# Kernel optimization log

Measured on AMD Instinct MI355X. Metric: run time of the kernel, lower is better.

The kernel has to match this reference:

```python
import jax, jax.numpy as jnp
import numpy as np

V, E, H2, T = 50000, 256, 512, 16  # vocab, embed, hidden_dim, tagset
H = H2 // 2                        # per-direction hidden
START, STOP = 14, 15
NEG = -10000.0


def setup_inputs() -> dict:
    key = jax.random.key(0)
    ks = jax.random.split(key, 13)
    s = 0.08
    tokens = jax.random.randint(ks[0], (32, 512), 0, V)
    embed_table = jax.random.normal(ks[1], (V, E), jnp.float32)
    Wi_f = jax.random.normal(ks[2], (4 * H, E), jnp.float32) * s
    Wh_f = jax.random.normal(ks[3], (4 * H, H), jnp.float32) * s
    bi_f = jnp.zeros((4 * H,), jnp.float32)
    bh_f = jnp.zeros((4 * H,), jnp.float32)
    Wi_b = jax.random.normal(ks[4], (4 * H, E), jnp.float32) * s
    Wh_b = jax.random.normal(ks[5], (4 * H, H), jnp.float32) * s
    bi_b = jnp.zeros((4 * H,), jnp.float32)
    bh_b = jnp.zeros((4 * H,), jnp.float32)
    Wt = jax.random.normal(ks[6], (T, H2), jnp.float32) * s
    bt = jnp.zeros((T,), jnp.float32)
    trans = jax.random.normal(ks[7], (T, T), jnp.float32)
    trans = trans.at[START, :].set(NEG).at[:, STOP].set(NEG)
    return {"tokens": tokens, "embed_table": embed_table,
            "Wi_f": Wi_f, "Wh_f": Wh_f, "bi_f": bi_f, "bh_f": bh_f,
            "Wi_b": Wi_b, "Wh_b": Wh_b, "bi_b": bi_b, "bh_b": bh_b,
            "Wt": Wt, "bt": bt, "transitions": trans}


def _lstm_dir(x, Wi, Wh, bi, bh, reverse=False):
    # x: [S, B, E] -> h seq [S, B, H], PyTorch gate order i,f,g,o
    S, B, _ = x.shape
    xs = x[::-1] if reverse else x
    pre = jnp.einsum('sbe,ge->sbg', xs, Wi) + bi + bh  # precompute input GEMM

    def step(carry, z_t):
        h, c = carry
        z = z_t + h @ Wh.T  # [B, 4H]
        i, f, g, o = jnp.split(z, 4, axis=-1)
        c = jax.nn.sigmoid(f) * c + jax.nn.sigmoid(i) * jnp.tanh(g)
        h = jax.nn.sigmoid(o) * jnp.tanh(c)
        return (h, c), h

    h0 = jnp.zeros((B, H), x.dtype)
    _, hs = jax.lax.scan(step, (h0, h0), pre)
    return hs[::-1] if reverse else hs


def reference(tokens, embed_table, Wi_f, Wh_f, bi_f, bh_f,
              Wi_b, Wh_b, bi_b, bh_b, Wt, bt, transitions):
    x = embed_table[tokens]                # [B, S, E]
    x = jnp.transpose(x, (1, 0, 2))        # [S, B, E] seq-first like nn.LSTM
    hf = _lstm_dir(x, Wi_f, Wh_f, bi_f, bh_f, reverse=False)
    hb = _lstm_dir(x, Wi_b, Wh_b, bi_b, bh_b, reverse=True)
    feats = jnp.concatenate([hf, hb], axis=-1)           # [S, B, 2H]
    emissions = jnp.einsum('sbh,th->sbt', feats, Wt) + bt  # [S, B, T]

    B = tokens.shape[0]
    alpha0 = jnp.full((B, T), NEG, jnp.float32).at[:, START].set(0.0)

    def crf_step(alpha, emit_t):
        # alpha: [B, T_prev]; transitions[next, prev]; emit_t: [B, T_next]
        scores = alpha[:, None, :] + transitions[None, :, :] + emit_t[:, :, None]
        return jax.nn.logsumexp(scores, axis=2), None

    alpha, _ = jax.lax.scan(crf_step, alpha0, emissions)
    log_Z = jax.nn.logsumexp(alpha + transitions[STOP][None, :], axis=1)  # [B]
    return log_Z
```

## Files before the change

kernel.cpp:

```cpp
#include <hip/hip_runtime.h>
#include <hip/hip_bf16.h>
#include <stdint.h>

typedef __attribute__((ext_vector_type(4))) float f32x4;
typedef __attribute__((ext_vector_type(8))) short bf16x8;

#define SENT 0xFFFFFFFFFFFFFFFFULL

#define WS_XBF   0u
#define WS_WIR   8388608u
#define WS_BIAS  9437184u
#define WS_PRE   9445376u
#define WS_HALL  76554240u
#define WS_CTL   93364224u
#define WS_EMIS  93368320u
#define WS_CHK   94416896u

__device__ __forceinline__ unsigned short f2bf(float x) {
    union { float f; unsigned int u; } v; v.f = x;
    return (unsigned short)((v.u + 0x7FFFu + ((v.u >> 16) & 1u)) >> 16);
}
__device__ __forceinline__ float bf2f(unsigned short b) {
    union { float f; unsigned int u; } v; v.u = ((unsigned int)b) << 16; return v.f;
}
__device__ __forceinline__ unsigned int pack2(float a, float b) {
    return (unsigned int)f2bf(a) | ((unsigned int)f2bf(b) << 16);
}
__device__ __forceinline__ float sigf(float x)  { return 1.0f / (1.0f + __expf(-x)); }
__device__ __forceinline__ float tanhf_(float x){ return 1.0f - 2.0f / (__expf(2.0f * x) + 1.0f); }

__global__ __launch_bounds__(256) void k_prep(
    const int* __restrict__ tokens, const float* __restrict__ embed,
    const float* __restrict__ Wi_f, const float* __restrict__ Wi_b,
    const float* __restrict__ bi_f, const float* __restrict__ bh_f,
    const float* __restrict__ bi_b, const float* __restrict__ bh_b,
    char* __restrict__ ws)
{
    int blk = blockIdx.x, tid = threadIdx.x;
    unsigned short* xbf  = (unsigned short*)(ws + WS_XBF);
    unsigned short* wir  = (unsigned short*)(ws + WS_WIR);
    float* biasr         = (float*)(ws + WS_BIAS);
    if (blk < 2048) {
        int rr = tid >> 5, cc = tid & 31;
        int r = blk * 8 + rr;
        int s = r >> 5, b = r & 31;
        int tok = tokens[b * 512 + s];
        int k = cc * 8;
        const float* src = embed + (size_t)tok * 256 + k;
        float4 a = *(const float4*)src;
        float4 c = *(const float4*)(src + 4);
        uint4 o; o.x = pack2(a.x, a.y); o.y = pack2(a.z, a.w);
        o.z = pack2(c.x, c.y); o.w = pack2(c.z, c.w);
        *(uint4*)(xbf + (size_t)r * 256 + k) = o;
    } else if (blk < 2304) {
        int rr = tid >> 5, cc = tid & 31;
        int rowp = (blk - 2048) * 8 + rr;
        int dir = rowp >> 10, q = rowp & 1023;
        int j = q >> 8, rs = q & 255;
        int g = rs >> 6, hl = rs & 63;
        int srow = g * 256 + j * 64 + hl;
        const float* W = dir ? Wi_b : Wi_f;
        int k = cc * 8;
        const float* src = W + (size_t)srow * 256 + k;
        float4 a = *(const float4*)src;
        float4 c = *(const float4*)(src + 4);
        uint4 o; o.x = pack2(a.x, a.y); o.y = pack2(a.z, a.w);
        o.z = pack2(c.x, c.y); o.w = pack2(c.z, c.w);
        *(uint4*)(wir + (size_t)rowp * 256 + k) = o;
        if (cc == 0)
            biasr[rowp] = dir ? (bi_b[srow] + bh_b[srow]) : (bi_f[srow] + bh_f[srow]);
    } else {
        if (blk == 2304 && tid < 16)
            ((unsigned int*)(ws + WS_CTL))[tid] = 0u;
        size_t g = (size_t)(blk - 2304) * 256 + tid;
        uint4* hall4 = (uint4*)(ws + WS_HALL);
        const unsigned int NF = 0xFFFFFFFFu;
        for (size_t u = g; u < 1050624u; u += 65536u) {
            size_t slot = (u >> 10) % 513u;
            uint4 val;
            if (slot == 0) { val.x = 0u; val.y = 0u; val.z = 0u; val.w = 0u; }
            else           { val.x = NF; val.y = NF; val.z = NF; val.w = NF; }
            hall4[u] = val;
        }
    }
}

__global__ __launch_bounds__(256) void k_pregemm(char* __restrict__ ws)
{
    __shared__ unsigned short Asb[128 * 136];
    __shared__ unsigned short Bsb[64 * 136];
    const unsigned short* xbf = (const unsigned short*)(ws + WS_XBF);
    const unsigned short* wir = (const unsigned short*)(ws + WS_WIR);
    const float* biasr        = (const float*)(ws + WS_BIAS);
    unsigned short* pre       = (unsigned short*)(ws + WS_PRE);
    int blk = blockIdx.x, tid = threadIdx.x;
    int mb = blk >> 5, nb = blk & 31;
    int Mbase = mb * 128, Nbase = nb * 64;
    int w = tid >> 6, l = tid & 63, col = l & 15, quad = l >> 4;
    f32x4 acc[4][2];
    #pragma unroll
    for (int a = 0; a < 4; ++a)
        #pragma unroll
        for (int b = 0; b < 2; ++b) acc[a][b] = (f32x4){0.f, 0.f, 0.f, 0.f};

    for (int kh = 0; kh < 2; ++kh) {
        __syncthreads();
        #pragma unroll
        for (int i = 0; i < 8; ++i) {
            int c = tid + i * 256;
            int row = c >> 4, c16 = c & 15;
            uint4 v = *(const uint4*)(xbf + ((size_t)(Mbase + row) * 256 + kh * 128 + c16 * 8));
            *(uint4*)(Asb + row * 136 + c16 * 8) = v;
        }
        #pragma unroll
        for (int i = 0; i < 4; ++i) {
            int c = tid + i * 256;
            int row = c >> 4, c16 = c & 15;
            uint4 v = *(const uint4*)(wir + ((size_t)(Nbase + row) * 256 + kh * 128 + c16 * 8));
            *(uint4*)(Bsb + row * 136 + c16 * 8) = v;
        }
        __syncthreads();
        int mhalf = w >> 1, nh = w & 1;
        #pragma unroll
        for (int kt = 0; kt < 4; ++kt) {
            bf16x8 bfr[2];
            #pragma unroll
            for (int nn = 0; nn < 2; ++nn)
                bfr[nn] = *(const bf16x8*)(Bsb + (16 * (nh * 2 + nn) + col) * 136 + kt * 32 + quad * 8);
            #pragma unroll
            for (int mm = 0; mm < 4; ++mm) {
                bf16x8 afr = *(const bf16x8*)(Asb + (16 * (mhalf * 4 + mm) + col) * 136 + kt * 32 + quad * 8);
                #pragma unroll
                for (int nn = 0; nn < 2; ++nn)
                    acc[mm][nn] = __builtin_amdgcn_mfma_f32_16x16x32_bf16(afr, bfr[nn], acc[mm][nn], 0, 0, 0);
            }
        }
    }
    #pragma unroll
    for (int mm = 0; mm < 4; ++mm) {
        int m_t = (w >> 1) * 4 + mm;
        int s = (Mbase >> 5) + (m_t >> 1);
        int bhalf = m_t & 1;
        #pragma unroll
        for (int nn = 0; nn < 2; ++nn) {
            int ncol = Nbase + 16 * ((w & 1) * 2 + nn) + col;
            int dir = ncol >> 10, j = (ncol >> 8) & 3, r = ncol & 255;
            int g = r >> 6, hl16 = (r >> 4) & 3;
            int tidp = (bhalf * 4 + hl16) * 64 + l;
            float bv = biasr[ncol];
            f32x4 a = acc[mm][nn];
            uint2 o;
            o.x = pack2(a[0] + bv, a[1] + bv);
            o.y = pack2(a[2] + bv, a[3] + bv);
            size_t off = (((size_t)(dir * 512 + s) * 4 + j) * 512 + tidp) * 16 + g * 4;
            *(uint2*)(pre + off) = o;
        }
    }
}

__global__ __launch_bounds__(512, 2) void k_rec(
    const float* __restrict__ Wh_f, const float* __restrict__ Wh_b, char* __restrict__ ws)
{
    __shared__ unsigned short hbuf[32 * 264];
    __shared__ unsigned short hst[8 * 16 * 20];
    __shared__ int sRole;
    int tid = threadIdx.x;

    if (tid == 0) {
        int xcd;
        asm volatile("s_getreg_b32 %0, hwreg(HW_REG_XCC_ID)" : "=s"(xcd));
        xcd &= 7;
        unsigned int* ctl = (unsigned int*)(ws + WS_CTL);
        unsigned int slot = __hip_atomic_fetch_add(&ctl[xcd], 1u,
                              __ATOMIC_RELAXED, __HIP_MEMORY_SCOPE_AGENT);
        int role = -1;
        if (slot < 8u) {
            if (slot == 7u) {
                unsigned int expv = 0u;
                __hip_atomic_compare_exchange_strong(&ctl[8], &expv, (unsigned int)(xcd + 1),
                    __ATOMIC_RELAXED, __ATOMIC_RELAXED, __HIP_MEMORY_SCOPE_AGENT);
            }
            unsigned int ts; long gc = 0;
            do {
                ts = __hip_atomic_fetch_add(&ctl[8], 0u,
                        __ATOMIC_RELAXED, __HIP_MEMORY_SCOPE_AGENT);
            } while (ts == 0u && ++gc < (1L << 26));
            if (ts == (unsigned int)(xcd + 1)) role = (int)slot;
        }
        sRole = role;
    }
    __syncthreads();
    int role = sRole;
    if (role < 0) return;
    int dir = role >> 2, j = role & 3;

    int w = tid >> 6, l = tid & 63, col = l & 15, quad = l >> 4;
    int m = w >> 2, hl16 = w & 3;
    const float* Wh = dir ? Wh_b : Wh_f;
    const unsigned short* pre = (const unsigned short*)(ws + WS_PRE);
    unsigned short* hall      = (unsigned short*)(ws + WS_HALL);

    bf16x8 wf[4][8];
    #pragma unroll
    for (int g = 0; g < 4; ++g) {
        int grow = g * 256 + j * 64 + hl16 * 16 + col;
        #pragma unroll
        for (int kt = 0; kt < 8; ++kt) {
            const float* src = Wh + (size_t)grow * 256 + kt * 32 + quad * 8;
            float4 x0 = *(const float4*)src;
            float4 x1 = *(const float4*)(src + 4);
            bf16x8 f;
            f[0] = (short)f2bf(x0.x); f[1] = (short)f2bf(x0.y);
            f[2] = (short)f2bf(x0.z); f[3] = (short)f2bf(x0.w);
            f[4] = (short)f2bf(x1.x); f[5] = (short)f2bf(x1.y);
            f[6] = (short)f2bf(x1.z); f[7] = (short)f2bf(x1.w);
            wf[g][kt] = f;
        }
    }
    for (int u = tid; u < 1280; u += 512) ((unsigned int*)hst)[u] = 0;
    __syncthreads();

    float cst[4] = {0.f, 0.f, 0.f, 0.f};
    size_t hbase_u = (size_t)dir * 513 * 8192;
    int row0 = tid >> 6, c8 = tid & 63;
    bool ownl = (c8 >= j * 16) && (c8 < j * 16 + 16);

    for (int st = 0; st < 512; ++st) {
        int s = dir ? (511 - st) : st;
        const uint4* pp = (const uint4*)(pre + ((((size_t)(dir * 512 + s)) * 4 + j) * 512 + tid) * 16);
        uint4 p0 = pp[0], p1 = pp[1];

        unsigned short* hsl = hall + hbase_u + (size_t)st * 8192;
        unsigned long long v[4];
        if (ownl) {
            int lc = c8 * 4 - j * 64;
            int hl = lc >> 4, c4 = lc & 15;
            #pragma unroll
            for (int i = 0; i < 4; ++i) {
                int row = row0 + i * 8;
                int wp = (row >> 4) * 4 + hl, r_in = row & 15;
                v[i] = *(const unsigned long long*)(hst + wp * 320 + r_in * 20 + c4);
            }
        } else {
            #pragma unroll
            for (int i = 0; i < 4; ++i) {
                unsigned long long expv = SENT;
                __hip_atomic_compare_exchange_strong(
                    (unsigned long long*)(hsl + (size_t)(tid + i * 512) * 4), &expv, SENT,
                    __ATOMIC_RELAXED, __ATOMIC_RELAXED, __HIP_MEMORY_SCOPE_WORKGROUP);
                v[i] = expv;
            }
            bool pend = (v[0] == SENT) | (v[1] == SENT) | (v[2] == SENT) | (v[3] == SENT);
            int rnd = 0;
            while (pend && rnd < 65536) {
                #pragma unroll
                for (int i = 0; i < 4; ++i) {
                    if (v[i] == SENT) {
                        unsigned long long expv = SENT;
                        __hip_atomic_compare_exchange_strong(
                            (unsigned long long*)(hsl + (size_t)(tid + i * 512) * 4), &expv, SENT,
                            __ATOMIC_RELAXED, __ATOMIC_RELAXED, __HIP_MEMORY_SCOPE_WORKGROUP);
                        v[i] = expv;
                    }
                }
                pend = (v[0] == SENT) | (v[1] == SENT) | (v[2] == SENT) | (v[3] == SENT);
                ++rnd;
            }
        }
        #pragma unroll
        for (int i = 0; i < 4; ++i)
            *(unsigned long long*)(hbuf + (row0 + i * 8) * 264 + c8 * 4) = v[i];
        __syncthreads();

        f32x4 acc[4];
        #pragma unroll
        for (int g = 0; g < 4; ++g) acc[g] = (f32x4){0.f, 0.f, 0.f, 0.f};
        #pragma unroll
        for (int kt = 0; kt < 8; ++kt) {
            bf16x8 af = *(const bf16x8*)(hbuf + (m * 16 + col) * 264 + kt * 32 + quad * 8);
            #pragma unroll
            for (int g = 0; g < 4; ++g)
                acc[g] = __builtin_amdgcn_mfma_f32_16x16x32_bf16(af, wf[g][kt], acc[g], 0, 0, 0);
        }
        unsigned int pw[8] = {p0.x, p0.y, p0.z, p0.w, p1.x, p1.y, p1.z, p1.w};
        float z[4][4];
        #pragma unroll
        for (int g = 0; g < 4; ++g) {
            #pragma unroll
            for (int r2 = 0; r2 < 2; ++r2) {
                unsigned int u = pw[g * 2 + r2];
                z[g][r2 * 2]     = acc[g][r2 * 2]     + bf2f((unsigned short)(u & 0xffff));
                z[g][r2 * 2 + 1] = acc[g][r2 * 2 + 1] + bf2f((unsigned short)(u >> 16));
            }
        }
        unsigned short hb16[4];
        #pragma unroll
        for (int r = 0; r < 4; ++r) {
            float ci = sigf(z[1][r]) * cst[r] + sigf(z[0][r]) * tanhf_(z[2][r]);
            cst[r] = ci;
            hb16[r] = f2bf(sigf(z[3][r]) * tanhf_(ci));
        }
        unsigned short* hw = hst + w * 320;
        #pragma unroll
        for (int r = 0; r < 4; ++r) hw[(quad * 4 + r) * 20 + col] = hb16[r];
        int rrow = l >> 2, cpart = l & 3;
        unsigned long long hv = *(const unsigned long long*)(hw + rrow * 20 + cpart * 4);
        size_t dsto = hbase_u + (size_t)(st + 1) * 8192 + (size_t)(m * 16 + rrow) * 256
                    + j * 64 + hl16 * 16 + cpart * 4;
        (void)__hip_atomic_exchange((unsigned long long*)(hall + dsto), hv,
                                    __ATOMIC_RELAXED, __HIP_MEMORY_SCOPE_WORKGROUP);
        __syncthreads();
    }
}

__global__ __launch_bounds__(256) void k_emis(
    const float* __restrict__ Wt, const float* __restrict__ bt, char* __restrict__ ws)
{
    __shared__ float WtL[16 * 528];
    __shared__ unsigned short hrow[16 * 536];
    __shared__ float btL[16];
    int blk = blockIdx.x, tid = threadIdx.x;
    int sbb = blk * 16;
    int s = sbb >> 5, bbase = sbb & 31;
    const unsigned short* hall = (const unsigned short*)(ws + WS_HALL);
    float* emis = (float*)(ws + WS_EMIS);
    #pragma unroll
    for (int i = 0; i < 8; ++i) {
        int c = tid + i * 256;
        int trow = c >> 7, c128 = c & 127;
        float4 v = *(const float4*)(Wt + (size_t)trow * 512 + c128 * 4);
        *(float4*)(WtL + trow * 528 + c128 * 4) = v;
    }
    #pragma unroll
    for (int i = 0; i < 4; ++i) {
        int c = tid + i * 256;
        int row = c >> 6, c6 = c & 63, half = c6 >> 5, c16 = c6 & 31;
        size_t base = half == 0 ? (size_t)(s + 1) * 8192 : ((size_t)513 + (512 - s)) * 8192;
        uint4 v = *(const uint4*)(hall + base + (size_t)(bbase + row) * 256 + c16 * 8);
        *(uint4*)(hrow + row * 536 + half * 256 + c16 * 8) = v;
    }
    if (tid < 16) btL[tid] = bt[tid];
    __syncthreads();
    int t = tid >> 4, i = tid & 15;
    float acc = btL[t];
    const float* wrow = WtL + t * 528;
    const unsigned short* hr = hrow + i * 536;
    #pragma unroll 8
    for (int k = 0; k < 512; k += 4) {
        uint2 hu = *(const uint2*)(hr + k);
        float4 wv = *(const float4*)(wrow + k);
        acc += bf2f((unsigned short)(hu.x & 0xffff)) * wv.x
             + bf2f((unsigned short)(hu.x >> 16))    * wv.y
             + bf2f((unsigned short)(hu.y & 0xffff)) * wv.z
             + bf2f((unsigned short)(hu.y >> 16))    * wv.w;
    }
    emis[((size_t)(bbase + i) * 512 + s) * 16 + t] = acc;
}

__global__ __launch_bounds__(256) void k_crfc(const float* __restrict__ trans, char* __restrict__ ws)
{
    __shared__ float trL[16 * 17];
    __shared__ float est[16 * 16];
    __shared__ float Pb[2][16 * 17];
    int blk = blockIdx.x, tid = threadIdx.x;
    int b = blk >> 5, c = blk & 31;
    int t = tid >> 4, p = tid & 15;
    const float* emis = (const float*)(ws + WS_EMIS);
    float* chk = (float*)(ws + WS_CHK);
    trL[t * 17 + p] = trans[t * 16 + p];
    est[t * 16 + p] = emis[((size_t)b * 512 + c * 16 + t) * 16 + p];
    __syncthreads();
    float tr[16];
    #pragma unroll
    for (int q = 0; q < 16; ++q) tr[q] = trL[t * 17 + q];
    float out = trL[t * 17 + p] + est[0 * 16 + t];
    Pb[0][t * 17 + p] = out;
    __syncthreads();
    int cur = 0;
    for (int si = 1; si < 16; ++si) {
        float v[16]; float mx = -3.0e38f;
        #pragma unroll
        for (int q = 0; q < 16; ++q) { v[q] = tr[q] + Pb[cur][q * 17 + p]; mx = fmaxf(mx, v[q]); }
        float ss = 0.f;
        #pragma unroll
        for (int q = 0; q < 16; ++q) ss += __expf(v[q] - mx);
        out = est[si * 16 + t] + mx + __logf(ss);
        Pb[1 - cur][t * 17 + p] = out;
        __syncthreads();
        cur = 1 - cur;
    }
    chk[(size_t)(b * 32 + c) * 256 + t * 16 + p] = out;
}

__global__ __launch_bounds__(256) void k_crff(
    const float* __restrict__ trans, char* __restrict__ ws, float* __restrict__ out)
{
    __shared__ float Cst[16 * 17];
    __shared__ float Pb[2][16 * 17];
    __shared__ float af[16];
    int b = blockIdx.x, tid = threadIdx.x;
    int t = tid >> 4, p = tid & 15;
    const float* chk = (const float*)(ws + WS_CHK);
    Pb[0][t * 17 + p] = chk[(size_t)(b * 32) * 256 + t * 16 + p];
    __syncthreads();
    int cur = 0;
    for (int ci = 1; ci < 32; ++ci) {
        Cst[t * 17 + p] = chk[(size_t)(b * 32 + ci) * 256 + t * 16 + p];
        __syncthreads();
        float v[16]; float mx = -3.0e38f;
        #pragma unroll
        for (int q = 0; q < 16; ++q) { v[q] = Cst[t * 17 + q] + Pb[cur][q * 17 + p]; mx = fmaxf(mx, v[q]); }
        float ss = 0.f;
        #pragma unroll
        for (int q = 0; q < 16; ++q) ss += __expf(v[q] - mx);
        float outv = mx + __logf(ss);
        Pb[1 - cur][t * 17 + p] = outv;
        __syncthreads();
        cur = 1 - cur;
    }
    float vfin = Pb[cur][t * 17 + p] + ((p == 14) ? 0.0f : -10000.0f);
    Cst[t * 17 + p] = vfin;
    __syncthreads();
    if (tid < 16) {
        float mx = -3.0e38f;
        for (int q = 0; q < 16; ++q) mx = fmaxf(mx, Cst[tid * 17 + q]);
        float ss = 0.f;
        for (int q = 0; q < 16; ++q) ss += __expf(Cst[tid * 17 + q] - mx);
        af[tid] = mx + __logf(ss) + trans[15 * 16 + tid];
    }
    __syncthreads();
    if (tid == 0) {
        float mx = -3.0e38f;
        for (int q = 0; q < 16; ++q) mx = fmaxf(mx, af[q]);
        float ss = 0.f;
        for (int q = 0; q < 16; ++q) ss += __expf(af[q] - mx);
        out[b] = mx + __logf(ss);
    }
}

extern "C" void kernel_launch(void* const* d_in, const int* in_sizes, int n_in,
                              void* d_out, int out_size, void* d_ws, size_t ws_size,
                              hipStream_t stream)
{
    const int*   tokens = (const int*)d_in[0];
    const float* embed  = (const float*)d_in[1];
    const float* Wi_f   = (const float*)d_in[2];
    const float* Wh_f   = (const float*)d_in[3];
    const float* bi_f   = (const float*)d_in[4];
    const float* bh_f   = (const float*)d_in[5];
    const float* Wi_b   = (const float*)d_in[6];
    const float* Wh_b   = (const float*)d_in[7];
    const float* bi_b   = (const float*)d_in[8];
    const float* bh_b   = (const float*)d_in[9];
    const float* Wt     = (const float*)d_in[10];
    const float* bt     = (const float*)d_in[11];
    const float* trans  = (const float*)d_in[12];
    char* ws = (char*)d_ws;
    float* out = (float*)d_out;

    hipLaunchKernelGGL(k_prep, dim3(2560), dim3(256), 0, stream,
                       tokens, embed, Wi_f, Wi_b, bi_f, bh_f, bi_b, bh_b, ws);
    hipLaunchKernelGGL(k_pregemm, dim3(4096), dim3(256), 0, stream, ws);
    hipLaunchKernelGGL(k_rec, dim3(128), dim3(512), 0, stream, Wh_f, Wh_b, ws);
    hipLaunchKernelGGL(k_emis, dim3(1024), dim3(256), 0, stream, Wt, bt, ws);
    hipLaunchKernelGGL(k_crfc, dim3(1024), dim3(256), 0, stream, trans, ws);
    hipLaunchKernelGGL(k_crff, dim3(32), dim3(256), 0, stream, trans, ws, out);
}
```

Baseline: 1.596 ms.

## Replace per-element sentinel polling with per-block step flags in recurrent LSTM

The recurrent LSTM kernel used to poll every hidden-state element of other blocks with atomic compare-exchange until its sentinel cleared. It now has each block publish a single flag per step after storing its hidden slice with plain stores, and consumers poll only the three peer flags before reading h with ordinary loads. This cuts the atomic traffic on the serial critical path. The flag uses relaxed, workgroup-scope atomics with no release/acquire fence, so the ordering between the data stores and the flag is not guaranteed across CUs and a reader could see stale values.

```diff
diff --git a/kernel.cpp b/kernel.cpp
--- a/kernel.cpp
+++ b/kernel.cpp
@@ -15,6 +15,7 @@
 #define WS_CTL   93364224u
 #define WS_EMIS  93368320u
 #define WS_CHK   94416896u
+#define WS_FLG   WS_CHK
 
 __device__ __forceinline__ unsigned short f2bf(float x) {
     union { float f; unsigned int u; } v; v.f = x;
@@ -72,6 +73,10 @@
     } else {
         if (blk == 2304 && tid < 16)
             ((unsigned int*)(ws + WS_CTL))[tid] = 0u;
+        if (blk == 2305) {
+            unsigned int* flg = (unsigned int*)(ws + WS_FLG);
+            for (int u = tid; u < 2 * 513 * 4 * 16; u += 256) flg[u] = 0u;
+        }
         size_t g = (size_t)(blk - 2304) * 256 + tid;
         uint4* hall4 = (uint4*)(ws + WS_HALL);
         const unsigned int NF = 0xFFFFFFFFu;
@@ -199,6 +204,7 @@
     const float* Wh = dir ? Wh_b : Wh_f;
     const unsigned short* pre = (const unsigned short*)(ws + WS_PRE);
     unsigned short* hall      = (unsigned short*)(ws + WS_HALL);
+    unsigned int* flags       = (unsigned int*)(ws + WS_FLG);
 
     bf16x8 wf[4][8];
     #pragma unroll
@@ -224,6 +230,7 @@
     size_t hbase_u = (size_t)dir * 513 * 8192;
     int row0 = tid >> 6, c8 = tid & 63;
     bool ownl = (c8 >= j * 16) && (c8 < j * 16 + 16);
+    int pollj = (l < 4 && l != j) ? l : -1;
 
     for (int st = 0; st < 512; ++st) {
         int s = dir ? (511 - st) : st;
@@ -231,6 +238,23 @@
         uint4 p0 = pp[0], p1 = pp[1];
 
         unsigned short* hsl = hall + hbase_u + (size_t)st * 8192;
+
+        if (st > 0) {
+            unsigned int* fl = flags + ((size_t)(dir * 513 + st)) * 64;
+            int got = (pollj < 0) ? 1 : 0;
+            int rnd = 0;
+            while (!__all(got)) {
+                if (!got) {
+                    unsigned int expv = 0u;
+                    __hip_atomic_compare_exchange_strong(fl + pollj * 16, &expv, 0u,
+                        __ATOMIC_RELAXED, __ATOMIC_RELAXED, __HIP_MEMORY_SCOPE_WORKGROUP);
+                    got = (expv != 0u) ? 1 : 0;
+                }
+                if (++rnd > (1 << 20)) break;
+            }
+            asm volatile("" ::: "memory");
+        }
+
         unsigned long long v[4];
         if (ownl) {
             int lc = c8 * 4 - j * 64;
@@ -243,29 +267,8 @@
             }
         } else {
             #pragma unroll
-            for (int i = 0; i < 4; ++i) {
-                unsigned long long expv = SENT;
-                __hip_atomic_compare_exchange_strong(
-                    (unsigned long long*)(hsl + (size_t)(tid + i * 512) * 4), &expv, SENT,
-                    __ATOMIC_RELAXED, __ATOMIC_RELAXED, __HIP_MEMORY_SCOPE_WORKGROUP);
-                v[i] = expv;
-            }
-            bool pend = (v[0] == SENT) | (v[1] == SENT) | (v[2] == SENT) | (v[3] == SENT);
-            int rnd = 0;
-            while (pend && rnd < 65536) {
-                #pragma unroll
-                for (int i = 0; i < 4; ++i) {
-                    if (v[i] == SENT) {
-                        unsigned long long expv = SENT;
-                        __hip_atomic_compare_exchange_strong(
-                            (unsigned long long*)(hsl + (size_t)(tid + i * 512) * 4), &expv, SENT,
-                            __ATOMIC_RELAXED, __ATOMIC_RELAXED, __HIP_MEMORY_SCOPE_WORKGROUP);
-                        v[i] = expv;
-                    }
-                }
-                pend = (v[0] == SENT) | (v[1] == SENT) | (v[2] == SENT) | (v[3] == SENT);
-                ++rnd;
-            }
+            for (int i = 0; i < 4; ++i)
+                v[i] = *(const unsigned long long*)(hsl + (size_t)(tid + i * 512) * 4);
         }
         #pragma unroll
         for (int i = 0; i < 4; ++i)
@@ -307,9 +310,11 @@
         unsigned long long hv = *(const unsigned long long*)(hw + rrow * 20 + cpart * 4);
         size_t dsto = hbase_u + (size_t)(st + 1) * 8192 + (size_t)(m * 16 + rrow) * 256
                     + j * 64 + hl16 * 16 + cpart * 4;
-        (void)__hip_atomic_exchange((unsigned long long*)(hall + dsto), hv,
-                                    __ATOMIC_RELAXED, __HIP_MEMORY_SCOPE_WORKGROUP);
-        __syncthreads();
+        *(unsigned long long*)(hall + dsto) = hv;
+        __syncthreads();
+        if (tid == 0)
+            (void)__hip_atomic_exchange(flags + ((size_t)(dir * 513 + st + 1)) * 64 + j * 16, 1u,
+                                        __ATOMIC_RELAXED, __HIP_MEMORY_SCOPE_WORKGROUP);
     }
 }
 
```

After: 1.814 ms. 1.14x slower.
